# Kernel optimization log

Hardware: AMD Instinct MI355X
Metric: run time of the kernel (lower is better)

## Reference

```python
import jax, jax.numpy as jnp
import numpy as np

N, IN_FEAT, OUT_FEAT = 1_000_000, 128, 128


def setup_inputs() -> dict:
    key = jax.random.key(0)
    k_x, k_m, k_w, k_b = jax.random.split(key, 4)
    x = jax.random.normal(k_x, (N, IN_FEAT), dtype=jnp.float32)
    amask = jax.random.bernoulli(k_m, 0.5, (N,))  # bool mask over rows
    # nn.Linear default init ~ U(-1/sqrt(in), 1/sqrt(in)); bias scaled by 0.001
    bound = 1.0 / np.sqrt(IN_FEAT)
    W = jax.random.uniform(k_w, (OUT_FEAT, IN_FEAT), minval=-bound, maxval=bound, dtype=jnp.float32)
    b = jax.random.uniform(k_b, (OUT_FEAT,), minval=-bound, maxval=bound, dtype=jnp.float32) * 0.001
    return {"x": x, "amask": amask, "W": W, "b": b}


def reference(x, amask, W, b):
    # Original: gather masked rows -> linear (+Identity act) -> scatter into zeros.
    # Equivalent fixed-shape math: dense linear, then zero out unmasked rows.
    y = x @ W.T + b  # [N, out_feat]
    return jnp.where(amask[:, None], y, jnp.zeros((), dtype=y.dtype))
```

## Files before the change

kernel.cpp:

```cpp
#include <hip/hip_runtime.h>
#include <stdint.h>
#include <stddef.h>


typedef __attribute__((ext_vector_type(8))) short short8;
typedef __attribute__((ext_vector_type(4))) float f32x4;

__device__ __forceinline__ unsigned short f2bf(float f) {
    union { float f; unsigned int u; } v; v.f = f;
    unsigned int u = v.u;
    unsigned int r = (u + 0x7FFFu + ((u >> 16) & 1u)) >> 16;
    return (unsigned short)r;
}

__device__ __forceinline__ short8 pack8(float4 lo, float4 hi) {
    short8 r;
    r[0] = (short)f2bf(lo.x); r[1] = (short)f2bf(lo.y);
    r[2] = (short)f2bf(lo.z); r[3] = (short)f2bf(lo.w);
    r[4] = (short)f2bf(hi.x); r[5] = (short)f2bf(hi.y);
    r[6] = (short)f2bf(hi.z); r[7] = (short)f2bf(hi.w);
    return r;
}

__global__ __launch_bounds__(256, 2)
void masked_linear_kernel(const float* __restrict__ x,
                          const int* __restrict__ amask,
                          const float* __restrict__ W,
                          const float* __restrict__ bias,
                          float* __restrict__ out,
                          int n_tiles, int n_waves)
{
    const int lane = threadIdx.x & 63;
    const int wid  = blockIdx.x * (blockDim.x >> 6) + (threadIdx.x >> 6);
    const int ln   = lane & 15;
    const int kg   = lane >> 4;

    short8 wf[8][4];
    float  bv[8];
#pragma unroll
    for (int t = 0; t < 8; ++t) {
        bv[t] = bias[t * 16 + ln];
        const float* wr = W + (t * 16 + ln) * 128 + kg * 8;
#pragma unroll
        for (int s = 0; s < 4; ++s) {
            const float4* p = reinterpret_cast<const float4*>(wr + s * 32);
            wf[t][s] = pack8(p[0], p[1]);
        }
    }

    for (int tile = wid; tile < n_tiles; tile += n_waves) {
        const int r0   = tile << 4;
        const int arow = r0 + ln;
        const bool m   = amask[arow] != 0;
        const int4 smask =
            *reinterpret_cast<const int4*>(amask + r0 + (kg << 2));

        const float* xr = x + (size_t)arow * 128 + kg * 8;
        short8 a[4];
#pragma unroll
        for (int s = 0; s < 4; ++s) {
            float4 lo = make_float4(0.f, 0.f, 0.f, 0.f);
            float4 hi = make_float4(0.f, 0.f, 0.f, 0.f);
            if (m) {
                const float4* p = reinterpret_cast<const float4*>(xr + s * 32);
                lo = p[0]; hi = p[1];
            }
            a[s] = pack8(lo, hi);
        }

        f32x4 acc[8];
#pragma unroll
        for (int t = 0; t < 8; ++t) {
            f32x4 v = {bv[t], bv[t], bv[t], bv[t]};
            acc[t] = v;
        }
#pragma unroll
        for (int s = 0; s < 4; ++s)
#pragma unroll
            for (int t = 0; t < 8; ++t)
                acc[t] = __builtin_amdgcn_mfma_f32_16x16x32_bf16(
                             a[s], wf[t][s], acc[t], 0, 0, 0);

        float* orow = out + (size_t)(r0 + (kg << 2)) * 128 + ln;
        const int km[4] = {smask.x, smask.y, smask.z, smask.w};
#pragma unroll
        for (int r = 0; r < 4; ++r) {
            const bool keep = km[r] != 0;
            float* op = orow + r * 128;
#pragma unroll
            for (int t = 0; t < 8; ++t)
                op[t * 16] = keep ? acc[t][r] : 0.0f;
        }
    }
}

extern "C" void kernel_launch(void* const* d_in, const int* in_sizes, int n_in,
                              void* d_out, int out_size, void* d_ws, size_t ws_size,
                              hipStream_t stream) {
    const float* x     = (const float*)d_in[0];
    const int*   amask = (const int*)d_in[1];
    const float* W     = (const float*)d_in[2];
    const float* b     = (const float*)d_in[3];
    float*       out   = (float*)d_out;

    const int n_rows  = in_sizes[1];
    const int n_tiles = n_rows >> 4;
    const int blocks  = 512;
    const int n_waves = blocks * 4;

    hipLaunchKernelGGL(masked_linear_kernel, dim3(blocks), dim3(256), 0, stream,
                       x, amask, W, b, out, n_tiles, n_waves);
}
```

Measured before the change: 793.2 us.

## Stage bf16 weight fragments in LDS, raise occupancy, use nontemporal output stores

```diff
diff --git a/kernel.cpp b/kernel.cpp
--- a/kernel.cpp
+++ b/kernel.cpp
@@ -13,16 +13,16 @@
     return (unsigned short)r;
 }
 
-__device__ __forceinline__ short8 pack8(float4 lo, float4 hi) {
+__device__ __forceinline__ short8 pack8(f32x4 lo, f32x4 hi) {
     short8 r;
-    r[0] = (short)f2bf(lo.x); r[1] = (short)f2bf(lo.y);
-    r[2] = (short)f2bf(lo.z); r[3] = (short)f2bf(lo.w);
-    r[4] = (short)f2bf(hi.x); r[5] = (short)f2bf(hi.y);
-    r[6] = (short)f2bf(hi.z); r[7] = (short)f2bf(hi.w);
+    r[0] = (short)f2bf(lo[0]); r[1] = (short)f2bf(lo[1]);
+    r[2] = (short)f2bf(lo[2]); r[3] = (short)f2bf(lo[3]);
+    r[4] = (short)f2bf(hi[0]); r[5] = (short)f2bf(hi[1]);
+    r[6] = (short)f2bf(hi[2]); r[7] = (short)f2bf(hi[3]);
     return r;
 }
 
-__global__ __launch_bounds__(256, 2)
+__global__ __launch_bounds__(256, 4)
 void masked_linear_kernel(const float* __restrict__ x,
                           const int* __restrict__ amask,
                           const float* __restrict__ W,
@@ -30,23 +30,26 @@
                           float* __restrict__ out,
                           int n_tiles, int n_waves)
 {
-    const int lane = threadIdx.x & 63;
-    const int wid  = blockIdx.x * (blockDim.x >> 6) + (threadIdx.x >> 6);
+    __shared__ short8 wlds[2048];
+
+    const int tid  = threadIdx.x;
+    const int lane = tid & 63;
+    const int wid  = blockIdx.x * (blockDim.x >> 6) + (tid >> 6);
     const int ln   = lane & 15;
     const int kg   = lane >> 4;
 
-    short8 wf[8][4];
-    float  bv[8];
+    for (int e = tid; e < 2048; e += 256) {
+        const int f = e >> 6, l = e & 63;
+        const int t = f >> 2, s = f & 3;
+        const int n  = t * 16 + (l & 15);
+        const int k0 = s * 32 + (l >> 4) * 8;
+        const f32x4* p = reinterpret_cast<const f32x4*>(W + n * 128 + k0);
+        wlds[e] = pack8(p[0], p[1]);
+    }
+    float bv[8];
 #pragma unroll
-    for (int t = 0; t < 8; ++t) {
-        bv[t] = bias[t * 16 + ln];
-        const float* wr = W + (t * 16 + ln) * 128 + kg * 8;
-#pragma unroll
-        for (int s = 0; s < 4; ++s) {
-            const float4* p = reinterpret_cast<const float4*>(wr + s * 32);
-            wf[t][s] = pack8(p[0], p[1]);
-        }
-    }
+    for (int t = 0; t < 8; ++t) bv[t] = bias[t * 16 + ln];
+    __syncthreads();
 
     for (int tile = wid; tile < n_tiles; tile += n_waves) {
         const int r0   = tile << 4;
@@ -59,10 +62,10 @@
         short8 a[4];
 #pragma unroll
         for (int s = 0; s < 4; ++s) {
-            float4 lo = make_float4(0.f, 0.f, 0.f, 0.f);
-            float4 hi = make_float4(0.f, 0.f, 0.f, 0.f);
+            f32x4 lo = {0.f, 0.f, 0.f, 0.f};
+            f32x4 hi = {0.f, 0.f, 0.f, 0.f};
             if (m) {
-                const float4* p = reinterpret_cast<const float4*>(xr + s * 32);
+                const f32x4* p = reinterpret_cast<const f32x4*>(xr + s * 32);
                 lo = p[0]; hi = p[1];
             }
             a[s] = pack8(lo, hi);
@@ -79,17 +82,17 @@
 #pragma unroll
             for (int t = 0; t < 8; ++t)
                 acc[t] = __builtin_amdgcn_mfma_f32_16x16x32_bf16(
-                             a[s], wf[t][s], acc[t], 0, 0, 0);
+                             a[s], wlds[(t * 4 + s) * 64 + lane], acc[t], 0, 0, 0);
 
         float* orow = out + (size_t)(r0 + (kg << 2)) * 128 + ln;
         const int km[4] = {smask.x, smask.y, smask.z, smask.w};
 #pragma unroll
         for (int r = 0; r < 4; ++r) {
             const bool keep = km[r] != 0;
-            float* op = orow + r * 128;
+            float* op = orow + (size_t)r * 128;
 #pragma unroll
             for (int t = 0; t < 8; ++t)
-                op[t * 16] = keep ? acc[t][r] : 0.0f;
+                __builtin_nontemporal_store(keep ? acc[t][r] : 0.0f, op + t * 16);
         }
     }
 }
@@ -105,7 +108,7 @@
 
     const int n_rows  = in_sizes[1];
     const int n_tiles = n_rows >> 4;
-    const int blocks  = 512;
+    const int blocks  = 1024;
     const int n_waves = blocks * 4;
 
     hipLaunchKernelGGL(masked_linear_kernel, dim3(blocks), dim3(256), 0, stream,
```

Result: slower. 998.3 us (+25.9%).
